# Kernel optimization log

Hardware: AMD Instinct MI355X
Metric: run time of the kernel (lower is better)

## Reference

```python
import jax, jax.numpy as jnp
import numpy as np

H = 7500.0
N, T, C = 64, 65536, 4


def setup_inputs() -> dict:
    key = jax.random.key(0)
    k1, k2, k3 = jax.random.split(key, 3)
    # predictions roughly in [0, h]
    output_rsd = jax.random.uniform(k1, (N, T, C), dtype=jnp.float32) * H
    # targets span [-0.25h, 1.25h] so >h, <0, in-range, and early bins are all hit
    u = jax.random.uniform(k2, (N, T, C), dtype=jnp.float32)
    target_rsd = (u * 1.5 - 0.25) * H
    z = jax.random.uniform(k3, (N, T, C), dtype=jnp.float32)
    target_rsd = jnp.where(z < 0.05, 0.0, target_rsd)
    return {"output_rsd": output_rsd, "target_rsd": target_rsd}


def _nanmean2(a, b):
    # nanmean over a stacked pair, elementwise
    va = ~jnp.isnan(a)
    vb = ~jnp.isnan(b)
    s = jnp.where(va, a, 0.0) + jnp.where(vb, b, 0.0)
    c = va.astype(a.dtype) + vb.astype(a.dtype)
    return jnp.where(c > 0, s / jnp.maximum(c, 1.0), jnp.nan)


def reference(output_rsd, target_rsd):
    h = jnp.float32(H)
    if target_rsd.ndim < 3:
        target_rsd = target_rsd[..., None]
    # clamp out-of-range targets to h (same as torch.where((t>h)|(t<0), h, t))
    t = jnp.where((target_rsd > h) | (target_rsd < 0), h, target_rsd)
    d = jnp.abs(output_rsd - t)  # [N, T, C]

    def masked_mean(mask):
        m = mask.astype(d.dtype)
        c = m.sum(axis=1)                  # [N, C]
        s = (d * m).sum(axis=1)            # [N, C]
        return jnp.where(c > 0, s / jnp.maximum(c, 1.0), jnp.nan)

    m_o = masked_mean(t == h)                          # over-horizon
    m_in = masked_mean((t < h) & (t > 0))              # in-horizon
    m_u = masked_mean(t == 0)                          # target exactly 0
    m_e = masked_mean((t < 0.1 * h) & (t > 0))         # early (<0.1h)

    in_comb = _nanmean2(m_u, m_in)   # per-(n,c) inMAE
    w = _nanmean2(m_o, in_comb)      # per-(n,c) wMAE

    wMAE = jnp.nanmean(w)
    inMAE = jnp.nanmean(in_comb)
    oMAE = jnp.nanmean(m_o)
    eMAE = jnp.nanmean(m_e)
    return (wMAE, inMAE, oMAE, eMAE)
```

## Files before the change

kernel.cpp:

```cpp
#include <hip/hip_runtime.h>
#include <math.h>

#define H_VAL   7500.0f
#define N_DIM   64
#define T_DIM   65536
#define C_DIM   4
#define BLOCKS_PER_N 32
#define THREADS 256
#define T_PER_BLOCK (T_DIM / BLOCKS_PER_N)
#define ITERS (T_PER_BLOCK / THREADS)

__device__ __forceinline__ float dev_nan() { return __uint_as_float(0x7fc00000u); }
__device__ __forceinline__ bool is_nan(float x) { return x != x; }

__global__ __launch_bounds__(THREADS) void mae_stage1(
        const float* __restrict__ outp, const float* __restrict__ tgtp,
        float* __restrict__ ws) {
    const int n = blockIdx.x / BLOCKS_PER_N;
    const int slice = blockIdx.x % BLOCKS_PER_N;
    const int t0 = slice * T_PER_BLOCK;
    const float h = H_VAL;
    const float eh = 0.1f * H_VAL;

    float acc[C_DIM][8];
    #pragma unroll
    for (int c = 0; c < C_DIM; ++c)
        #pragma unroll
        for (int k = 0; k < 8; ++k) acc[c][k] = 0.0f;

    const float4* o4 = reinterpret_cast<const float4*>(outp) + (size_t)n * T_DIM;
    const float4* t4 = reinterpret_cast<const float4*>(tgtp) + (size_t)n * T_DIM;

    #pragma unroll
    for (int it = 0; it < ITERS; ++it) {
        const int t = t0 + it * THREADS + (int)threadIdx.x;
        const float4 ov = o4[t];
        const float4 tv = t4[t];
        const float os[4] = {ov.x, ov.y, ov.z, ov.w};
        const float ts[4] = {tv.x, tv.y, tv.z, tv.w};
        #pragma unroll
        for (int c = 0; c < C_DIM; ++c) {
            const float traw = ts[c];
            const float tc = ((traw > h) || (traw < 0.0f)) ? h : traw;
            const float d = fabsf(os[c] - tc);
            const bool b_o  = (tc == h);
            const bool b_u  = (tc == 0.0f);
            const bool b_in = (tc < h) && (tc > 0.0f);
            const bool b_e  = (tc < eh) && (tc > 0.0f);
            acc[c][0] += b_o  ? d : 0.0f;  acc[c][1] += b_o  ? 1.0f : 0.0f;
            acc[c][2] += b_in ? d : 0.0f;  acc[c][3] += b_in ? 1.0f : 0.0f;
            acc[c][4] += b_u  ? d : 0.0f;  acc[c][5] += b_u  ? 1.0f : 0.0f;
            acc[c][6] += b_e  ? d : 0.0f;  acc[c][7] += b_e  ? 1.0f : 0.0f;
        }
    }

    #pragma unroll
    for (int c = 0; c < C_DIM; ++c) {
        #pragma unroll
        for (int k = 0; k < 8; ++k) {
            float v = acc[c][k];
            #pragma unroll
            for (int off = 32; off > 0; off >>= 1)
                v += __shfl_down(v, off, 64);
            acc[c][k] = v;
        }
    }

    __shared__ float lds[4][32];
    const int wave = threadIdx.x >> 6;
    const int lane = threadIdx.x & 63;
    if (lane == 0) {
        #pragma unroll
        for (int c = 0; c < C_DIM; ++c)
            #pragma unroll
            for (int k = 0; k < 8; ++k)
                lds[wave][c * 8 + k] = acc[c][k];
    }
    __syncthreads();
    if (threadIdx.x < 32) {
        const float v = lds[0][threadIdx.x] + lds[1][threadIdx.x] +
                        lds[2][threadIdx.x] + lds[3][threadIdx.x];
        atomicAdd(&ws[n * 32 + (int)threadIdx.x], v);
    }
}

__global__ __launch_bounds__(256) void mae_stage2(
        const float* __restrict__ ws, float* __restrict__ outp) {
    const int i = threadIdx.x;
    const int n = i >> 2, c = i & 3;
    const float* a = &ws[n * 32 + c * 8];

    const float m_o  = (a[1] > 0.0f) ? a[0] / a[1] : dev_nan();
    const float m_in = (a[3] > 0.0f) ? a[2] / a[3] : dev_nan();
    const float m_u  = (a[5] > 0.0f) ? a[4] / a[5] : dev_nan();
    const float m_e  = (a[7] > 0.0f) ? a[6] / a[7] : dev_nan();

    auto nm2 = [](float x, float y) {
        const bool vx = !is_nan(x), vy = !is_nan(y);
        const float s  = (vx ? x : 0.0f) + (vy ? y : 0.0f);
        const float cc = (vx ? 1.0f : 0.0f) + (vy ? 1.0f : 0.0f);
        return (cc > 0.0f) ? s / cc : dev_nan();
    };
    const float in_comb = nm2(m_u, m_in);
    const float w       = nm2(m_o, in_comb);

    float vals[4] = {w, in_comb, m_o, m_e};
    float sums[4], cnts[4];
    #pragma unroll
    for (int j = 0; j < 4; ++j) {
        const bool v = !is_nan(vals[j]);
        sums[j] = v ? vals[j] : 0.0f;
        cnts[j] = v ? 1.0f : 0.0f;
    }
    #pragma unroll
    for (int j = 0; j < 4; ++j) {
        #pragma unroll
        for (int off = 32; off > 0; off >>= 1) {
            sums[j] += __shfl_down(sums[j], off, 64);
            cnts[j] += __shfl_down(cnts[j], off, 64);
        }
    }
    __shared__ float ls[4][8];
    const int wave = threadIdx.x >> 6;
    const int lane = threadIdx.x & 63;
    if (lane == 0) {
        #pragma unroll
        for (int j = 0; j < 4; ++j) { ls[wave][j] = sums[j]; ls[wave][j + 4] = cnts[j]; }
    }
    __syncthreads();
    if (threadIdx.x == 0) {
        #pragma unroll
        for (int j = 0; j < 4; ++j) {
            const float s  = ls[0][j] + ls[1][j] + ls[2][j] + ls[3][j];
            const float cc = ls[0][j + 4] + ls[1][j + 4] + ls[2][j + 4] + ls[3][j + 4];
            outp[j] = (cc > 0.0f) ? s / cc : dev_nan();
        }
    }
}

extern "C" void kernel_launch(void* const* d_in, const int* in_sizes, int n_in,
                              void* d_out, int out_size, void* d_ws, size_t ws_size,
                              hipStream_t stream) {
    const float* out_rsd = (const float*)d_in[0];
    const float* tgt_rsd = (const float*)d_in[1];
    float* outv = (float*)d_out;
    float* ws = (float*)d_ws;

    hipMemsetAsync(ws, 0, N_DIM * 32 * sizeof(float), stream);

    mae_stage1<<<N_DIM * BLOCKS_PER_N, THREADS, 0, stream>>>(out_rsd, tgt_rsd, ws);
    mae_stage2<<<1, 256, 0, stream>>>(ws, outv);
}
```

Measured before the change: 37.77 us.

## Derive in-horizon stats algebraically, count via ballot, transpose-reduce sums

Cuts the per-element accumulators from 32 floats to 16 by deriving the in-horizon sum and count from totals minus the over-horizon and zero bins. Bin counts become wave-level ballot popcounts instead of per-lane float adds. The cross-lane reduction is replaced by a butterfly transpose-reduce that shares shuffles across the 16 values, and launch bounds now request higher occupancy. The main risks are float rounding from computing the in-horizon sum by subtraction, and the extra scalar ballot work in the inner loop.

```diff
diff --git a/kernel.cpp b/kernel.cpp
--- a/kernel.cpp
+++ b/kernel.cpp
@@ -2,9 +2,9 @@
 #include <math.h>
 
 #define H_VAL   7500.0f
+#define EH_VAL  750.0f
 #define N_DIM   64
 #define T_DIM   65536
-#define C_DIM   4
 #define BLOCKS_PER_N 32
 #define THREADS 256
 #define T_PER_BLOCK (T_DIM / BLOCKS_PER_N)
@@ -13,20 +13,21 @@
 __device__ __forceinline__ float dev_nan() { return __uint_as_float(0x7fc00000u); }
 __device__ __forceinline__ bool is_nan(float x) { return x != x; }
 
-__global__ __launch_bounds__(THREADS) void mae_stage1(
+__global__ __launch_bounds__(THREADS, 8) void mae_stage1(
         const float* __restrict__ outp, const float* __restrict__ tgtp,
         float* __restrict__ ws) {
     const int n = blockIdx.x / BLOCKS_PER_N;
     const int slice = blockIdx.x % BLOCKS_PER_N;
     const int t0 = slice * T_PER_BLOCK;
     const float h = H_VAL;
-    const float eh = 0.1f * H_VAL;
+    const float eh = EH_VAL;
 
-    float acc[C_DIM][8];
+    float v[16];
     #pragma unroll
-    for (int c = 0; c < C_DIM; ++c)
-        #pragma unroll
-        for (int k = 0; k < 8; ++k) acc[c][k] = 0.0f;
+    for (int i = 0; i < 16; ++i) v[i] = 0.0f;
+    int co[4] = {0, 0, 0, 0};
+    int cu[4] = {0, 0, 0, 0};
+    int ce[4] = {0, 0, 0, 0};
 
     const float4* o4 = reinterpret_cast<const float4*>(outp) + (size_t)n * T_DIM;
     const float4* t4 = reinterpret_cast<const float4*>(tgtp) + (size_t)n * T_DIM;
@@ -39,48 +40,67 @@
         const float os[4] = {ov.x, ov.y, ov.z, ov.w};
         const float ts[4] = {tv.x, tv.y, tv.z, tv.w};
         #pragma unroll
-        for (int c = 0; c < C_DIM; ++c) {
+        for (int c = 0; c < 4; ++c) {
             const float traw = ts[c];
-            const float tc = ((traw > h) || (traw < 0.0f)) ? h : traw;
+            const bool bo = (traw >= h) || (traw < 0.0f);
+            const float tc = bo ? h : traw;
             const float d = fabsf(os[c] - tc);
-            const bool b_o  = (tc == h);
-            const bool b_u  = (tc == 0.0f);
-            const bool b_in = (tc < h) && (tc > 0.0f);
-            const bool b_e  = (tc < eh) && (tc > 0.0f);
-            acc[c][0] += b_o  ? d : 0.0f;  acc[c][1] += b_o  ? 1.0f : 0.0f;
-            acc[c][2] += b_in ? d : 0.0f;  acc[c][3] += b_in ? 1.0f : 0.0f;
-            acc[c][4] += b_u  ? d : 0.0f;  acc[c][5] += b_u  ? 1.0f : 0.0f;
-            acc[c][6] += b_e  ? d : 0.0f;  acc[c][7] += b_e  ? 1.0f : 0.0f;
+            const bool bu = (traw == 0.0f);
+            const bool be = (traw > 0.0f) && (traw < eh);
+
+            v[c * 4 + 0] += d;
+            v[c * 4 + 1] += bo ? d : 0.0f;
+            v[c * 4 + 2] += bu ? d : 0.0f;
+            v[c * 4 + 3] += be ? d : 0.0f;
+
+            co[c] += __popcll(__ballot(bo));
+            cu[c] += __popcll(__ballot(bu));
+            ce[c] += __popcll(__ballot(be));
         }
     }
 
+    const int lane = threadIdx.x & 63;
     #pragma unroll
-    for (int c = 0; c < C_DIM; ++c) {
+    for (int r = 0; r < 4; ++r) {
+        const int dist = 1 << r;
+        const bool hi = (lane >> r) & 1;
+        const int cnt = 8 >> r;
         #pragma unroll
-        for (int k = 0; k < 8; ++k) {
-            float v = acc[c][k];
-            #pragma unroll
-            for (int off = 32; off > 0; off >>= 1)
-                v += __shfl_down(v, off, 64);
-            acc[c][k] = v;
+        for (int j = 0; j < cnt; ++j) {
+            const float send = hi ? v[j] : v[j + cnt];
+            const float recv = __shfl_xor(send, dist, 64);
+            v[j] = (hi ? v[j + cnt] : v[j]) + recv;
         }
     }
+    v[0] += __shfl_xor(v[0], 16, 64);
+    v[0] += __shfl_xor(v[0], 32, 64);
+    const int slot = ((lane & 1) << 3) | (((lane >> 1) & 1) << 2) |
+                     (((lane >> 2) & 1) << 1) | ((lane >> 3) & 1);
 
-    __shared__ float lds[4][32];
+    __shared__ float lsum[4][16];
+    __shared__ int   lcnt[4][12];
     const int wave = threadIdx.x >> 6;
-    const int lane = threadIdx.x & 63;
+    if (lane < 16) lsum[wave][slot] = v[0];
     if (lane == 0) {
         #pragma unroll
-        for (int c = 0; c < C_DIM; ++c)
-            #pragma unroll
-            for (int k = 0; k < 8; ++k)
-                lds[wave][c * 8 + k] = acc[c][k];
+        for (int c = 0; c < 4; ++c) {
+            lcnt[wave][c * 3 + 0] = co[c];
+            lcnt[wave][c * 3 + 1] = cu[c];
+            lcnt[wave][c * 3 + 2] = ce[c];
+        }
     }
     __syncthreads();
-    if (threadIdx.x < 32) {
-        const float v = lds[0][threadIdx.x] + lds[1][threadIdx.x] +
-                        lds[2][threadIdx.x] + lds[3][threadIdx.x];
-        atomicAdd(&ws[n * 32 + (int)threadIdx.x], v);
+    if (threadIdx.x < 16) {
+        const int i = threadIdx.x;
+        const float s = lsum[0][i] + lsum[1][i] + lsum[2][i] + lsum[3][i];
+        const int c = i >> 2, k = i & 3;
+        atomicAdd(&ws[n * 32 + c * 8 + k], s);
+    }
+    if (threadIdx.x < 12) {
+        const int i = threadIdx.x;
+        const int s = lcnt[0][i] + lcnt[1][i] + lcnt[2][i] + lcnt[3][i];
+        const int c = i / 3, k = i % 3;
+        atomicAdd(&ws[n * 32 + c * 8 + 4 + k], (float)s);
     }
 }
 
@@ -90,10 +110,15 @@
     const int n = i >> 2, c = i & 3;
     const float* a = &ws[n * 32 + c * 8];
 
-    const float m_o  = (a[1] > 0.0f) ? a[0] / a[1] : dev_nan();
-    const float m_in = (a[3] > 0.0f) ? a[2] / a[3] : dev_nan();
-    const float m_u  = (a[5] > 0.0f) ? a[4] / a[5] : dev_nan();
-    const float m_e  = (a[7] > 0.0f) ? a[6] / a[7] : dev_nan();
+    const float sum_all = a[0], sum_o = a[1], sum_u = a[2], sum_e = a[3];
+    const float cnt_o = a[4], cnt_u = a[5], cnt_e = a[6];
+    const float cnt_in = (float)T_DIM - cnt_o - cnt_u;
+    const float sum_in = sum_all - sum_o - sum_u;
+
+    const float m_o  = (cnt_o  > 0.0f) ? sum_o  / cnt_o  : dev_nan();
+    const float m_in = (cnt_in > 0.0f) ? sum_in / cnt_in : dev_nan();
+    const float m_u  = (cnt_u  > 0.0f) ? sum_u  / cnt_u  : dev_nan();
+    const float m_e  = (cnt_e  > 0.0f) ? sum_e  / cnt_e  : dev_nan();
 
     auto nm2 = [](float x, float y) {
         const bool vx = !is_nan(x), vy = !is_nan(y);
@@ -108,9 +133,9 @@
     float sums[4], cnts[4];
     #pragma unroll
     for (int j = 0; j < 4; ++j) {
-        const bool v = !is_nan(vals[j]);
-        sums[j] = v ? vals[j] : 0.0f;
-        cnts[j] = v ? 1.0f : 0.0f;
+        const bool valid = !is_nan(vals[j]);
+        sums[j] = valid ? vals[j] : 0.0f;
+        cnts[j] = valid ? 1.0f : 0.0f;
     }
     #pragma unroll
     for (int j = 0; j < 4; ++j) {
```

New measurement: 55.19 us. 46.1% more time.
